# Optimization experiments

Hardware: AMD Instinct MI355X
Metric: run time of the kernel (lower is better)

The kernel has to match this reference:

```python
import jax, jax.numpy as jnp
import numpy as np

M0, M1, M2 = 128, 64, 32            # multiplicities of 0e, 1o, 2e
NUM_IRREPS = M0 + M1 + M2           # 224
NODE_DIM = 128
SPH_DIM = M0 + 3 * M1 + 5 * M2      # 480
HIDDEN = 2 * NODE_DIM + NUM_IRREPS  # 480
N = 100000
EPS = 1e-5
SQ3 = float(np.sqrt(3.0))
SQ5 = float(np.sqrt(5.0))


def _split(x):
    s0 = x[:, :M0]                                   # [N,128]   l=0
    s1 = x[:, M0:M0 + 3 * M1].reshape(-1, M1, 3)     # [N,64,3]  l=1
    s2 = x[:, M0 + 3 * M1:].reshape(-1, M2, 5)       # [N,32,5]  l=2
    return s0, s1, s2


def _merge(s0, s1, s2):
    n = s0.shape[0]
    return jnp.concatenate([s0, s1.reshape(n, -1), s2.reshape(n, -1)], axis=-1)


def _o3_linear(s0, s1, s2, w0, w1, w2, b0):
    # e3nn o3.Linear: one path per l, element path-normalization 1/sqrt(mul_in); bias only on 0e
    y0 = s0 @ w0 / np.float32(np.sqrt(M0)) + b0
    y1 = jnp.einsum('nik,io->nok', s1, w1) / np.float32(np.sqrt(M1))
    y2 = jnp.einsum('nik,io->nok', s2, w2) / np.float32(np.sqrt(M2))
    return y0, y1, y2


def _o3_layernorm(s0, s1, s2, w, b):
    # equivariant layer norm: mean-center scalars only; RMS over (mul, components) per irrep type
    f0 = s0 - jnp.mean(s0, axis=1, keepdims=True)
    n0 = jnp.mean(f0 * f0, axis=1, keepdims=True)
    f0 = f0 * jax.lax.rsqrt(n0 + EPS) * w[:M0] + b
    n1 = jnp.mean(s1 * s1, axis=(1, 2))[:, None, None]
    f1 = s1 * jax.lax.rsqrt(n1 + EPS) * w[M0:M0 + M1][None, :, None]
    n2 = jnp.mean(s2 * s2, axis=(1, 2))[:, None, None]
    f2 = s2 * jax.lax.rsqrt(n2 + EPS) * w[M0 + M1:][None, :, None]
    return f0, f1, f2


def setup_inputs() -> dict:
    key = jax.random.key(0)
    ks = jax.random.split(key, 16)
    g = lambda k, shape: jax.random.normal(k, shape, jnp.float32)
    return {
        'x_scalar': g(ks[0], (N, NODE_DIM)),
        'x_spherical': g(ks[1], (N, SPH_DIM)),
        'ln_g': jnp.ones((NODE_DIM,), jnp.float32),
        'ln_b': jnp.zeros((NODE_DIM,), jnp.float32),
        'o3n_w': jnp.ones((NUM_IRREPS,), jnp.float32),
        'o3n_b': jnp.zeros((M0,), jnp.float32),
        'U_w0': g(ks[2], (M0, M0)), 'U_w1': g(ks[3], (M1, M1)), 'U_w2': g(ks[4], (M2, M2)),
        'U_b0': jnp.zeros((M0,), jnp.float32),
        'V_w0': g(ks[5], (M0, M0)), 'V_w1': g(ks[6], (M1, M1)), 'V_w2': g(ks[7], (M2, M2)),
        'V_b0': jnp.zeros((M0,), jnp.float32),
        'dot_w': g(ks[8], (NUM_IRREPS, NODE_DIM)) / np.float32(np.sqrt(NUM_IRREPS)),
        'mlp_w1': g(ks[9], (NODE_DIM + NUM_IRREPS, NODE_DIM)) / np.float32(np.sqrt(NODE_DIM + NUM_IRREPS)),
        'mlp_b1': jnp.zeros((NODE_DIM,), jnp.float32),
        'mlp_w2': g(ks[10], (NODE_DIM, HIDDEN)) / np.float32(np.sqrt(NODE_DIM)),
        'mlp_b2': jnp.zeros((HIDDEN,), jnp.float32),
    }


def reference(x_scalar, x_spherical, ln_g, ln_b, o3n_w, o3n_b,
              U_w0, U_w1, U_w2, U_b0, V_w0, V_w1, V_w2, V_b0,
              dot_w, mlp_w1, mlp_b1, mlp_w2, mlp_b2):
    # scalar layer norm
    mu = jnp.mean(x_scalar, axis=-1, keepdims=True)
    var = jnp.var(x_scalar, axis=-1, keepdims=True)
    scalar_in = (x_scalar - mu) * jax.lax.rsqrt(var + EPS) * ln_g + ln_b
    # equivariant layer norm on spherical features
    s0, s1, s2 = _split(x_spherical)
    s0, s1, s2 = _o3_layernorm(s0, s1, s2, o3n_w, o3n_b)
    U0, U1, U2 = _o3_linear(s0, s1, s2, U_w0, U_w1, U_w2, U_b0)
    V0, V1, V2 = _o3_linear(s0, s1, s2, V_w0, V_w1, V_w2, V_b0)
    # o3.Norm: per-irrep L2 norm -> [N, 224]
    inv = jnp.concatenate([jnp.abs(V0),
                           jnp.sqrt(jnp.sum(V1 * V1, axis=-1)),
                           jnp.sqrt(jnp.sum(V2 * V2, axis=-1))], axis=-1)
    mlp_in = jnp.concatenate([scalar_in, inv], axis=-1)          # [N, 352]
    h = jax.nn.silu(mlp_in @ mlp_w1 + mlp_b1)
    mlp_out = h @ mlp_w2 + mlp_b2                                # [N, 480]
    a_vv = mlp_out[:, :NUM_IRREPS]
    a_sv = mlp_out[:, NUM_IRREPS:NUM_IRREPS + NODE_DIM]
    a_ss = mlp_out[:, NUM_IRREPS + NODE_DIM:]
    # ElementwiseTensorProduct with 224x0e: per-irrep scalar gating (net factor 1)
    d0 = U0 * a_vv[:, :M0]
    d1 = U1 * a_vv[:, M0:M0 + M1, None]
    d2 = U2 * a_vv[:, M0 + M1:, None]
    # EquivariantDot (component-normalized uuu TP to 0e): dot / sqrt(2l+1)
    dot = jnp.concatenate([U0 * V0,
                           jnp.sum(U1 * V1, axis=-1) / SQ3,
                           jnp.sum(U2 * V2, axis=-1) / SQ5], axis=-1)
    inner = dot @ dot_w                                           # [N, 128]
    d_scalar = a_sv * inner + a_ss
    return x_scalar + d_scalar, x_spherical + _merge(d0, d1, d2)
```

## Files before the change

### kernel.cpp

```cpp
#include <hip/hip_runtime.h>
#include <stdint.h>

typedef unsigned short u16;
typedef __attribute__((ext_vector_type(2))) unsigned short u16x2;
typedef __attribute__((ext_vector_type(4))) unsigned short u16x4;
typedef __attribute__((ext_vector_type(8))) short s16x8;
typedef __attribute__((ext_vector_type(2))) float f32x2;
typedef __attribute__((ext_vector_type(4))) float f32x4;

#define NROWS 100000
#define RPB   16
#define NBLK  (NROWS / RPB)
#define NTHR  512

#define PF   488
#define PS   360
#define PH   136
#define PD   232
#define PAB  484
#define PIF  132

#define OFF_FIN   0
#define OFF_AOUT  0
#define OFF_SCB   15616
#define OFF_INNER 15616
#define OFF_DOTB  27136
#define OFF_HB    34560
#define OFF_BCOM  38912
#define ARENA_SZ  40640

#define B_UW0 0
#define B_UW1 16384
#define B_UW2 20480
#define B_VW0 21504
#define B_VW1 37888
#define B_VW2 41984
#define B_DW  43008
#define B_W1  71680
#define B_W2  116736
#define PACK_TOT 178176

__device__ inline float bf2f(u16 u) {
    union { uint32_t i; float f; } v; v.i = (uint32_t)u << 16; return v.f;
}
__device__ inline u16 f2bf(float f) {
    union { float f; uint32_t i; } v; v.f = f;
    return (u16)((v.i + 0x7fffu + ((v.i >> 16) & 1u)) >> 16);
}
__device__ inline float wsum32(float v) {
    #pragma unroll
    for (int m = 16; m >= 1; m >>= 1) v += __shfl_xor(v, m);
    return v;
}
__device__ inline bool detect_f32(const void* xs) {
    const u16 v = ((const u16*)xs)[threadIdx.x & 63];
    const float f = bf2f(v);
    return __any(!(fabsf(f) < 1e10f)) != 0;
}
__device__ inline float ldin(const void* p, size_t i, bool f32) {
    return f32 ? ((const float*)p)[i] : bf2f(((const u16*)p)[i]);
}
__device__ inline void stout(void* p, size_t i, float v, bool f32) {
    if (f32) ((float*)p)[i] = v; else ((u16*)p)[i] = f2bf(v);
}

struct Ptrs {
    const void *xs, *xp, *lng, *lnb, *o3w, *o3b;
    const void *Uw0, *Uw1, *Uw2, *Ub0, *Vw0, *Vw1, *Vw2, *Vb0;
    const void *dw, *w1, *b1, *w2, *b2;
    const u16 *ws;
    void *out;
};

template<int KS, bool PACKED>
__device__ inline f32x4 mm_acc(const u16* A, int pitchA, const void* W, int D,
                               int tile, int lane, bool wf32)
{
    f32x4 acc = {0.f, 0.f, 0.f, 0.f};
    const int r = lane & 15, g = lane >> 4;
    const u16* arow = A + r * pitchA + g * 8;
    #pragma unroll
    for (int ks = 0; ks < KS; ++ks) {
        s16x8 a = *(const s16x8*)(arow + ks * 32);
        s16x8 b;
        if (PACKED) {
            b = *(const s16x8*)((const u16*)W + (((size_t)tile * KS + ks) * 64 + (size_t)lane) * 8);
        } else {
            union { u16 u[8]; s16x8 v; } bb;
            const int k0 = ks * 32 + g * 8, o = tile * 16 + r;
            #pragma unroll
            for (int j = 0; j < 8; ++j) {
                const size_t idx = (size_t)(k0 + j) * D + o;
                bb.u[j] = wf32 ? f2bf(((const float*)W)[idx]) : ((const u16*)W)[idx];
            }
            b = bb.v;
        }
        acc = __builtin_amdgcn_mfma_f32_16x16x32_bf16(a, b, acc, 0, 0, 0);
    }
    return acc;
}

template<int KS, bool PACKED, int TYPE>
__device__ inline void mm_tile(const u16* A, int pitchA, const void* W, int D,
                               int tile, int lane, float scale, const u16* bias,
                               void* outP, int outPitch, bool wf32)
{
    f32x4 acc = mm_acc<KS, PACKED>(A, pitchA, W, D, tile, lane, wf32);
    const int r = lane & 15, g = lane >> 4;
    const int o = tile * 16 + r;
    if (TYPE == 0) {
        const float bv = bias ? bf2f(bias[o]) : 0.f;
        #pragma unroll
        for (int q = 0; q < 4; ++q)
            ((u16*)outP)[(size_t)(g * 4 + q) * outPitch + o] = f2bf(acc[q] * scale + bv);
    } else if (TYPE == 1) {
        const float bv = bf2f(bias[o]);
        #pragma unroll
        for (int q = 0; q < 4; ++q) {
            float x = acc[q] + bv;
            ((u16*)outP)[(size_t)(g * 4 + q) * outPitch + o] = f2bf(x / (1.f + expf(-x)));
        }
    } else {
        #pragma unroll
        for (int q = 0; q < 4; ++q)
            ((float*)outP)[(size_t)(g * 4 + q) * outPitch + o] = acc[q];
    }
}

__global__ void pack_weights(Ptrs P, u16* ws)
{
    const bool wf32 = detect_f32(P.xs);
    const int gid = blockIdx.x * 256 + threadIdx.x;
    if (gid >= PACK_TOT) return;
    const int  base[10] = {B_UW0, B_UW1, B_UW2, B_VW0, B_VW1, B_VW2, B_DW, B_W1, B_W2, PACK_TOT};
    const int  Kd[9]    = {128, 64, 32, 128, 64, 32, 224, 352, 128};
    const void* srcs[9] = {P.Uw0, P.Uw1, P.Uw2, P.Vw0, P.Vw1, P.Vw2, P.dw, P.w1, P.w2};
    const int  Dstride[9] = {128, 64, 32, 128, 64, 32, 128, 128, 480};
    int m = 0;
    for (int i = 1; i < 9; ++i) if (gid >= base[i]) m = i;
    const int e = gid - base[m];
    const int j = e & 7, lane = (e >> 3) & 63, tk = e >> 9;
    const int Ks = Kd[m] >> 5;
    const int ks = tk % Ks, tile = tk / Ks;
    const int k = ks * 32 + ((lane >> 4) << 3) + j;
    const int o = tile * 16 + (lane & 15);
    const size_t idx = (size_t)k * Dstride[m] + o;
    ws[gid] = wf32 ? f2bf(((const float*)srcs[m])[idx]) : ((const u16*)srcs[m])[idx];
}

template<int DT>
__device__ inline void stage1_core(const Ptrs& P, u16* fin, u16* scb, int tid, int row0)
{
    const int rr = tid >> 5, l32 = tid & 31;
    const size_t row = (size_t)(row0 + rr);
    const u16*   xsb = (const u16*)P.xs + row * 128;
    const float* xsf = (const float*)P.xs + row * 128;
    const u16*   xpb = (const u16*)P.xp + row * 480;
    const float* xpf = (const float*)P.xp + row * 480;
    {
        float v[4];
        if (DT) { f32x4 u = *(const f32x4*)(xsf + l32 * 4); v[0]=u[0];v[1]=u[1];v[2]=u[2];v[3]=u[3]; }
        else    { u16x4 u = *(const u16x4*)(xsb + l32 * 4);
                  v[0]=bf2f(u[0]);v[1]=bf2f(u[1]);v[2]=bf2f(u[2]);v[3]=bf2f(u[3]); }
        float s  = v[0] + v[1] + v[2] + v[3];
        float s2 = v[0]*v[0] + v[1]*v[1] + v[2]*v[2] + v[3]*v[3];
        s = wsum32(s); s2 = wsum32(s2);
        const float mu = s * (1.f / 128.f);
        const float rs = 1.f / sqrtf(s2 * (1.f / 128.f) - mu * mu + 1e-5f);
        const int c = l32 * 4;
        #pragma unroll
        for (int j2 = 0; j2 < 4; ++j2)
            scb[rr * PS + c + j2] =
                f2bf((v[j2] - mu) * rs * ldin(P.lng, c + j2, DT) + ldin(P.lnb, c + j2, DT));
    }
    {
        float v[4];
        if (DT) { f32x4 u = *(const f32x4*)(xpf + l32 * 4); v[0]=u[0];v[1]=u[1];v[2]=u[2];v[3]=u[3]; }
        else    { u16x4 u = *(const u16x4*)(xpb + l32 * 4);
                  v[0]=bf2f(u[0]);v[1]=bf2f(u[1]);v[2]=bf2f(u[2]);v[3]=bf2f(u[3]); }
        float s  = v[0] + v[1] + v[2] + v[3];
        float s2 = v[0]*v[0] + v[1]*v[1] + v[2]*v[2] + v[3]*v[3];
        s = wsum32(s); s2 = wsum32(s2);
        const float mu = s * (1.f / 128.f);
        const float rs = 1.f / sqrtf(s2 * (1.f / 128.f) - mu * mu + 1e-5f);
        const int c = l32 * 4;
        #pragma unroll
        for (int j2 = 0; j2 < 4; ++j2)
            fin[rr * PF + c + j2] =
                f2bf((v[j2] - mu) * rs * ldin(P.o3w, c + j2, DT) + ldin(P.o3b, c + j2, DT));
    }
    {
        const int cb = l32 * 6;
        float w[6];
        if (DT) {
            f32x2 a0 = *(const f32x2*)(xpf + 128 + cb);
            f32x2 a1 = *(const f32x2*)(xpf + 128 + cb + 2);
            f32x2 a2 = *(const f32x2*)(xpf + 128 + cb + 4);
            w[0]=a0[0]; w[1]=a0[1]; w[2]=a1[0]; w[3]=a1[1]; w[4]=a2[0]; w[5]=a2[1];
        } else {
            u16x2 a0 = *(const u16x2*)(xpb + 128 + cb);
            u16x2 a1 = *(const u16x2*)(xpb + 128 + cb + 2);
            u16x2 a2 = *(const u16x2*)(xpb + 128 + cb + 4);
            w[0]=bf2f(a0[0]); w[1]=bf2f(a0[1]); w[2]=bf2f(a1[0]);
            w[3]=bf2f(a1[1]); w[4]=bf2f(a2[0]); w[5]=bf2f(a2[1]);
        }
        float ss = 0.f;
        #pragma unroll
        for (int j2 = 0; j2 < 6; ++j2) ss += w[j2] * w[j2];
        ss = wsum32(ss);
        const float rs = 1.f / sqrtf(ss * (1.f / 192.f) + 1e-5f);
        #pragma unroll
        for (int j2 = 0; j2 < 6; ++j2) {
            const int c = cb + j2, i = c / 3, k = c - 3 * i;
            fin[rr * PF + 128 + k * 64 + i] = f2bf(w[j2] * rs * ldin(P.o3w, 128 + i, DT));
        }
    }
    {
        const int cb = l32 * 5;
        float w[5];
        #pragma unroll
        for (int j2 = 0; j2 < 5; ++j2)
            w[j2] = DT ? xpf[320 + cb + j2] : bf2f(xpb[320 + cb + j2]);
        float ss = 0.f;
        #pragma unroll
        for (int j2 = 0; j2 < 5; ++j2) ss += w[j2] * w[j2];
        ss = wsum32(ss);
        const float rs = 1.f / sqrtf(ss * (1.f / 160.f) + 1e-5f);
        #pragma unroll
        for (int j2 = 0; j2 < 5; ++j2) {
            const int c = cb + j2, i = c / 5, k = c - 5 * i;
            fin[rr * PF + 320 + k * 32 + i] = f2bf(w[j2] * rs * ldin(P.o3w, 192 + i, DT));
        }
    }
}

template<bool PACKED>
__global__ __launch_bounds__(NTHR, 6) void xpainn_main(Ptrs P)
{
    __shared__ __align__(16) unsigned char arena[ARENA_SZ];
    u16*   fin    = (u16*)(arena + OFF_FIN);
    u16*   aoutB  = (u16*)(arena + OFF_AOUT);
    u16*   scb    = (u16*)(arena + OFF_SCB);
    float* innerF = (float*)(arena + OFF_INNER);
    u16*   dotb   = (u16*)(arena + OFF_DOTB);
    u16*   hb     = (u16*)(arena + OFF_HB);
    u16*   bcom   = (u16*)(arena + OFF_BCOM);

    const int tid = threadIdx.x;
    const int lane = tid & 63, wave = tid >> 6;
    const int r = lane & 15, g = lane >> 4;
    const int row0 = blockIdx.x * RPB;
    const bool isf32 = detect_f32(P.xs);

    for (int i = tid; i < 864; i += NTHR) {
        const void* src; int off;
        if (i < 128)      { src = P.Ub0; off = i; }
        else if (i < 256) { src = P.Vb0; off = i - 128; }
        else if (i < 384) { src = P.b1;  off = i - 256; }
        else              { src = P.b2;  off = i - 384; }
        bcom[i] = f2bf(ldin(src, off, isf32));
    }
    if (isf32) stage1_core<1>(P, fin, scb, tid, row0);
    else       stage1_core<0>(P, fin, scb, tid, row0);
    __syncthreads();

    float u0r[4];
    float uxr[5][4];
    {
        const int o = wave * 16 + r;
        f32x4 au = mm_acc<4, PACKED>(fin, PF,
            PACKED ? (const void*)(P.ws + B_UW0) : P.Uw0, 128, wave, lane, isf32);
        f32x4 av = mm_acc<4, PACKED>(fin, PF,
            PACKED ? (const void*)(P.ws + B_VW0) : P.Vw0, 128, wave, lane, isf32);
        const float bu = bf2f(bcom[o]), bv = bf2f(bcom[128 + o]);
        #pragma unroll
        for (int q = 0; q < 4; ++q) {
            const float U = au[q] * 0.08838834764831845f + bu;
            const float V = av[q] * 0.08838834764831845f + bv;
            u0r[q] = U;
            const int row = g * 4 + q;
            scb[row * PS + 128 + o]  = f2bf(fabsf(V));
            dotb[row * PD + o]       = f2bf(U * V);
        }
    }
    if (wave < 4) {
        const int tt = wave, o = tt * 16 + r;
        float sv[4] = {0.f,0.f,0.f,0.f}, suv[4] = {0.f,0.f,0.f,0.f};
        #pragma unroll
        for (int ch = 0; ch < 3; ++ch) {
            f32x4 au = mm_acc<2, PACKED>(fin + 128 + 64 * ch, PF,
                PACKED ? (const void*)(P.ws + B_UW1) : P.Uw1, 64, tt, lane, isf32);
            f32x4 av = mm_acc<2, PACKED>(fin + 128 + 64 * ch, PF,
                PACKED ? (const void*)(P.ws + B_VW1) : P.Vw1, 64, tt, lane, isf32);
            #pragma unroll
            for (int q = 0; q < 4; ++q) {
                const float U = au[q] * 0.125f, V = av[q] * 0.125f;
                uxr[ch][q] = U; sv[q] += V * V; suv[q] += U * V;
            }
        }
        #pragma unroll
        for (int q = 0; q < 4; ++q) {
            const int row = g * 4 + q;
            scb[row * PS + 256 + o]  = f2bf(sqrtf(sv[q]));
            dotb[row * PD + 128 + o] = f2bf(suv[q] * 0.5773502691896258f);
        }
    } else if (wave < 6) {
        const int tt = wave - 4, o = tt * 16 + r;
        float sv[4] = {0.f,0.f,0.f,0.f}, suv[4] = {0.f,0.f,0.f,0.f};
        #pragma unroll
        for (int ch = 0; ch < 5; ++ch) {
            f32x4 au = mm_acc<1, PACKED>(fin + 320 + 32 * ch, PF,
                PACKED ? (const void*)(P.ws + B_UW2) : P.Uw2, 32, tt, lane, isf32);
            f32x4 av = mm_acc<1, PACKED>(fin + 320 + 32 * ch, PF,
                PACKED ? (const void*)(P.ws + B_VW2) : P.Vw2, 32, tt, lane, isf32);
            #pragma unroll
            for (int q = 0; q < 4; ++q) {
                const float U = au[q] * 0.17677669529663687f, V = av[q] * 0.17677669529663687f;
                uxr[ch][q] = U; sv[q] += V * V; suv[q] += U * V;
            }
        }
        #pragma unroll
        for (int q = 0; q < 4; ++q) {
            const int row = g * 4 + q;
            scb[row * PS + 320 + o]  = f2bf(sqrtf(sv[q]));
            dotb[row * PD + 192 + o] = f2bf(suv[q] * 0.4472135954999579f);
        }
    }
    __syncthreads();

    mm_tile<11, PACKED, 1>(scb, PS, PACKED ? (const void*)(P.ws + B_W1) : P.w1,
                           128, wave, lane, 1.f, bcom + 256, hb, PH, isf32);
    __syncthreads();

    for (int ti = wave; ti < 38; ti += 8) {
        if (ti < 30)
            mm_tile<4, PACKED, 0>(hb, PH, PACKED ? (const void*)(P.ws + B_W2) : P.w2,
                                  480, ti, lane, 1.f, bcom + 384, aoutB, PAB, isf32);
        else
            mm_tile<7, PACKED, 2>(dotb, PD, PACKED ? (const void*)(P.ws + B_DW) : P.dw,
                                  128, ti - 30, lane, 1.f, nullptr, innerF, PIF, isf32);
    }
    __syncthreads();

    {
        const int idx = tid;
        const int r2 = idx >> 5, c4 = (idx & 31) * 4;
        const size_t gb = (size_t)(row0 + r2) * 128 + c4;
        const u16x4 asv = *(const u16x4*)(aoutB + r2 * PAB + 224 + c4);
        const u16x4 ass = *(const u16x4*)(aoutB + r2 * PAB + 352 + c4);
        const f32x4 inn = *(const f32x4*)(innerF + r2 * PIF + c4);
        if (isf32) {
            const f32x4 xs = *(const f32x4*)((const float*)P.xs + gb);
            f32x4 o;
            #pragma unroll
            for (int j = 0; j < 4; ++j) o[j] = xs[j] + bf2f(asv[j]) * inn[j] + bf2f(ass[j]);
            *(f32x4*)((float*)P.out + gb) = o;
        } else {
            const u16x4 xs = *(const u16x4*)((const u16*)P.xs + gb);
            u16x4 o;
            #pragma unroll
            for (int j = 0; j < 4; ++j) o[j] = f2bf(bf2f(xs[j]) + bf2f(asv[j]) * inn[j] + bf2f(ass[j]));
            *(u16x4*)((u16*)P.out + gb) = o;
        }
    }
    {
        const size_t ob = (size_t)NROWS * 128;
        const int o = wave * 16 + r;
        #pragma unroll
        for (int q = 0; q < 4; ++q) {
            const int row = g * 4 + q;
            const size_t gr = (size_t)(row0 + row) * 480;
            const float av = bf2f(aoutB[row * PAB + o]);
            stout(P.out, ob + gr + o, ldin(P.xp, gr + o, isf32) + u0r[q] * av, isf32);
        }
        if (wave < 4) {
            const int i = wave * 16 + r;
            #pragma unroll
            for (int q = 0; q < 4; ++q) {
                const int row = g * 4 + q;
                const size_t gr = (size_t)(row0 + row) * 480;
                const float av = bf2f(aoutB[row * PAB + 128 + i]);
                #pragma unroll
                for (int ch = 0; ch < 3; ++ch) {
                    const size_t c = 128 + 3 * i + ch;
                    stout(P.out, ob + gr + c, ldin(P.xp, gr + c, isf32) + uxr[ch][q] * av, isf32);
                }
            }
        } else if (wave < 6) {
            const int i = (wave - 4) * 16 + r;
            #pragma unroll
            for (int q = 0; q < 4; ++q) {
                const int row = g * 4 + q;
                const size_t gr = (size_t)(row0 + row) * 480;
                const float av = bf2f(aoutB[row * PAB + 192 + i]);
                #pragma unroll
                for (int ch = 0; ch < 5; ++ch) {
                    const size_t c = 320 + 5 * i + ch;
                    stout(P.out, ob + gr + c, ldin(P.xp, gr + c, isf32) + uxr[ch][q] * av, isf32);
                }
            }
        }
    }
}

extern "C" void kernel_launch(void* const* d_in, const int* in_sizes, int n_in,
                              void* d_out, int out_size, void* d_ws, size_t ws_size,
                              hipStream_t stream)
{
    Ptrs P;
    P.xs  = d_in[0];  P.xp  = d_in[1];
    P.lng = d_in[2];  P.lnb = d_in[3];
    P.o3w = d_in[4];  P.o3b = d_in[5];
    P.Uw0 = d_in[6];  P.Uw1 = d_in[7];
    P.Uw2 = d_in[8];  P.Ub0 = d_in[9];
    P.Vw0 = d_in[10]; P.Vw1 = d_in[11];
    P.Vw2 = d_in[12]; P.Vb0 = d_in[13];
    P.dw  = d_in[14]; P.w1  = d_in[15];
    P.b1  = d_in[16]; P.w2  = d_in[17];
    P.b2  = d_in[18];
    P.ws  = (const u16*)d_ws;
    P.out = d_out;

    const bool packed = (ws_size >= (size_t)PACK_TOT * sizeof(u16));
    if (packed) {
        pack_weights<<<(PACK_TOT + 255) / 256, 256, 0, stream>>>(P, (u16*)d_ws);
        xpainn_main<true><<<NBLK, NTHR, 0, stream>>>(P);
    } else {
        xpainn_main<false><<<NBLK, NTHR, 0, stream>>>(P);
    }
}
```

Measured before the change: 244.3 us.

## Process 32 rows per block and reuse weight fragments across two row groups

Doubles rows per block from 16 to 32, splitting the shared-memory arena into two 16-row groups. Each weight B-fragment is now loaded into registers once and applied to both row groups' MFMAs, halving weight-load traffic per row. The costs are double the LDS footprint (about 79.5KB), a launch-bounds occupancy hint lowered from 6 to 4, and more live registers for the per-group U values, which may reduce latency hiding. 100000 rows still divide evenly into 32-row blocks.

```diff
diff --git a/kernel.cpp b/kernel.cpp
--- a/kernel.cpp
+++ b/kernel.cpp
@@ -9,7 +9,7 @@
 typedef __attribute__((ext_vector_type(4))) float f32x4;
 
 #define NROWS 100000
-#define RPB   16
+#define RPB   32
 #define NBLK  (NROWS / RPB)
 #define NTHR  512
 
@@ -19,15 +19,21 @@
 #define PD   232
 #define PAB  484
 #define PIF  132
+#define FIN_RG  (16 * PF)
+#define SCB_RG  (16 * PS)
+#define HB_RG   (16 * PH)
+#define DOT_RG  (16 * PD)
+#define AOUT_RG (16 * PAB)
+#define INN_RG  (16 * PIF)
 
 #define OFF_FIN   0
 #define OFF_AOUT  0
-#define OFF_SCB   15616
-#define OFF_INNER 15616
-#define OFF_DOTB  27136
-#define OFF_HB    34560
-#define OFF_BCOM  38912
-#define ARENA_SZ  40640
+#define OFF_SCB   31232
+#define OFF_INNER 31232
+#define OFF_DOTB  54272
+#define OFF_HB    69120
+#define OFF_BCOM  77824
+#define ARENA_SZ  79552
 
 #define B_UW0 0
 #define B_UW1 16384
@@ -73,57 +79,52 @@
 };
 
 template<int KS, bool PACKED>
-__device__ inline f32x4 mm_acc(const u16* A, int pitchA, const void* W, int D,
-                               int tile, int lane, bool wf32)
-{
-    f32x4 acc = {0.f, 0.f, 0.f, 0.f};
-    const int r = lane & 15, g = lane >> 4;
-    const u16* arow = A + r * pitchA + g * 8;
+__device__ inline void load_b(const void* W, int D, int tile, int lane, bool wf32, s16x8* bfr)
+{
     #pragma unroll
     for (int ks = 0; ks < KS; ++ks) {
-        s16x8 a = *(const s16x8*)(arow + ks * 32);
-        s16x8 b;
         if (PACKED) {
-            b = *(const s16x8*)((const u16*)W + (((size_t)tile * KS + ks) * 64 + (size_t)lane) * 8);
+            bfr[ks] = *(const s16x8*)((const u16*)W + (((size_t)tile * KS + ks) * 64 + (size_t)lane) * 8);
         } else {
             union { u16 u[8]; s16x8 v; } bb;
-            const int k0 = ks * 32 + g * 8, o = tile * 16 + r;
+            const int k0 = ks * 32 + ((lane >> 4) << 3), o = tile * 16 + (lane & 15);
             #pragma unroll
             for (int j = 0; j < 8; ++j) {
                 const size_t idx = (size_t)(k0 + j) * D + o;
                 bb.u[j] = wf32 ? f2bf(((const float*)W)[idx]) : ((const u16*)W)[idx];
             }
-            b = bb.v;
-        }
-        acc = __builtin_amdgcn_mfma_f32_16x16x32_bf16(a, b, acc, 0, 0, 0);
+            bfr[ks] = bb.v;
+        }
+    }
+}
+
+template<int KS>
+__device__ inline f32x4 acc_ab(const u16* A, int pitchA, int lane, const s16x8* bfr)
+{
+    f32x4 acc = {0.f, 0.f, 0.f, 0.f};
+    const u16* arow = A + (lane & 15) * pitchA + (lane >> 4) * 8;
+    #pragma unroll
+    for (int ks = 0; ks < KS; ++ks) {
+        s16x8 a = *(const s16x8*)(arow + ks * 32);
+        acc = __builtin_amdgcn_mfma_f32_16x16x32_bf16(a, bfr[ks], acc, 0, 0, 0);
     }
     return acc;
 }
 
-template<int KS, bool PACKED, int TYPE>
-__device__ inline void mm_tile(const u16* A, int pitchA, const void* W, int D,
-                               int tile, int lane, float scale, const u16* bias,
-                               void* outP, int outPitch, bool wf32)
-{
-    f32x4 acc = mm_acc<KS, PACKED>(A, pitchA, W, D, tile, lane, wf32);
+template<int KS, bool PACKED>
+__device__ inline void mm_silu(const u16* A, int pitchA, const void* W, int D,
+                               int tile, int lane, const u16* bias, u16* outH, bool wf32)
+{
+    s16x8 bfr[KS];
+    load_b<KS, PACKED>(W, D, tile, lane, wf32, bfr);
+    f32x4 acc = acc_ab<KS>(A, pitchA, lane, bfr);
     const int r = lane & 15, g = lane >> 4;
     const int o = tile * 16 + r;
-    if (TYPE == 0) {
-        const float bv = bias ? bf2f(bias[o]) : 0.f;
-        #pragma unroll
-        for (int q = 0; q < 4; ++q)
-            ((u16*)outP)[(size_t)(g * 4 + q) * outPitch + o] = f2bf(acc[q] * scale + bv);
-    } else if (TYPE == 1) {
-        const float bv = bf2f(bias[o]);
-        #pragma unroll
-        for (int q = 0; q < 4; ++q) {
-            float x = acc[q] + bv;
-            ((u16*)outP)[(size_t)(g * 4 + q) * outPitch + o] = f2bf(x / (1.f + expf(-x)));
-        }
-    } else {
-        #pragma unroll
-        for (int q = 0; q < 4; ++q)
-            ((float*)outP)[(size_t)(g * 4 + q) * outPitch + o] = acc[q];
+    const float bv = bf2f(bias[o]);
+    #pragma unroll
+    for (int q = 0; q < 4; ++q) {
+        float x = acc[q] + bv;
+        outH[(g * 4 + q) * PH + o] = f2bf(x / (1.f + expf(-x)));
     }
 }
 
@@ -149,93 +150,99 @@
 }
 
 template<int DT>
-__device__ inline void stage1_core(const Ptrs& P, u16* fin, u16* scb, int tid, int row0)
-{
-    const int rr = tid >> 5, l32 = tid & 31;
-    const size_t row = (size_t)(row0 + rr);
-    const u16*   xsb = (const u16*)P.xs + row * 128;
-    const float* xsf = (const float*)P.xs + row * 128;
-    const u16*   xpb = (const u16*)P.xp + row * 480;
-    const float* xpf = (const float*)P.xp + row * 480;
-    {
-        float v[4];
-        if (DT) { f32x4 u = *(const f32x4*)(xsf + l32 * 4); v[0]=u[0];v[1]=u[1];v[2]=u[2];v[3]=u[3]; }
-        else    { u16x4 u = *(const u16x4*)(xsb + l32 * 4);
-                  v[0]=bf2f(u[0]);v[1]=bf2f(u[1]);v[2]=bf2f(u[2]);v[3]=bf2f(u[3]); }
-        float s  = v[0] + v[1] + v[2] + v[3];
-        float s2 = v[0]*v[0] + v[1]*v[1] + v[2]*v[2] + v[3]*v[3];
-        s = wsum32(s); s2 = wsum32(s2);
-        const float mu = s * (1.f / 128.f);
-        const float rs = 1.f / sqrtf(s2 * (1.f / 128.f) - mu * mu + 1e-5f);
-        const int c = l32 * 4;
-        #pragma unroll
-        for (int j2 = 0; j2 < 4; ++j2)
-            scb[rr * PS + c + j2] =
-                f2bf((v[j2] - mu) * rs * ldin(P.lng, c + j2, DT) + ldin(P.lnb, c + j2, DT));
-    }
-    {
-        float v[4];
-        if (DT) { f32x4 u = *(const f32x4*)(xpf + l32 * 4); v[0]=u[0];v[1]=u[1];v[2]=u[2];v[3]=u[3]; }
-        else    { u16x4 u = *(const u16x4*)(xpb + l32 * 4);
-                  v[0]=bf2f(u[0]);v[1]=bf2f(u[1]);v[2]=bf2f(u[2]);v[3]=bf2f(u[3]); }
-        float s  = v[0] + v[1] + v[2] + v[3];
-        float s2 = v[0]*v[0] + v[1]*v[1] + v[2]*v[2] + v[3]*v[3];
-        s = wsum32(s); s2 = wsum32(s2);
-        const float mu = s * (1.f / 128.f);
-        const float rs = 1.f / sqrtf(s2 * (1.f / 128.f) - mu * mu + 1e-5f);
-        const int c = l32 * 4;
-        #pragma unroll
-        for (int j2 = 0; j2 < 4; ++j2)
-            fin[rr * PF + c + j2] =
-                f2bf((v[j2] - mu) * rs * ldin(P.o3w, c + j2, DT) + ldin(P.o3b, c + j2, DT));
-    }
-    {
-        const int cb = l32 * 6;
-        float w[6];
-        if (DT) {
-            f32x2 a0 = *(const f32x2*)(xpf + 128 + cb);
-            f32x2 a1 = *(const f32x2*)(xpf + 128 + cb + 2);
-            f32x2 a2 = *(const f32x2*)(xpf + 128 + cb + 4);
-            w[0]=a0[0]; w[1]=a0[1]; w[2]=a1[0]; w[3]=a1[1]; w[4]=a2[0]; w[5]=a2[1];
-        } else {
-            u16x2 a0 = *(const u16x2*)(xpb + 128 + cb);
-            u16x2 a1 = *(const u16x2*)(xpb + 128 + cb + 2);
-            u16x2 a2 = *(const u16x2*)(xpb + 128 + cb + 4);
-            w[0]=bf2f(a0[0]); w[1]=bf2f(a0[1]); w[2]=bf2f(a1[0]);
-            w[3]=bf2f(a1[1]); w[4]=bf2f(a2[0]); w[5]=bf2f(a2[1]);
-        }
-        float ss = 0.f;
-        #pragma unroll
-        for (int j2 = 0; j2 < 6; ++j2) ss += w[j2] * w[j2];
-        ss = wsum32(ss);
-        const float rs = 1.f / sqrtf(ss * (1.f / 192.f) + 1e-5f);
-        #pragma unroll
-        for (int j2 = 0; j2 < 6; ++j2) {
-            const int c = cb + j2, i = c / 3, k = c - 3 * i;
-            fin[rr * PF + 128 + k * 64 + i] = f2bf(w[j2] * rs * ldin(P.o3w, 128 + i, DT));
-        }
-    }
-    {
-        const int cb = l32 * 5;
-        float w[5];
-        #pragma unroll
-        for (int j2 = 0; j2 < 5; ++j2)
-            w[j2] = DT ? xpf[320 + cb + j2] : bf2f(xpb[320 + cb + j2]);
-        float ss = 0.f;
-        #pragma unroll
-        for (int j2 = 0; j2 < 5; ++j2) ss += w[j2] * w[j2];
-        ss = wsum32(ss);
-        const float rs = 1.f / sqrtf(ss * (1.f / 160.f) + 1e-5f);
-        #pragma unroll
-        for (int j2 = 0; j2 < 5; ++j2) {
-            const int c = cb + j2, i = c / 5, k = c - 5 * i;
-            fin[rr * PF + 320 + k * 32 + i] = f2bf(w[j2] * rs * ldin(P.o3w, 192 + i, DT));
+__device__ inline void stage1_core(const Ptrs& P, u16* fin0, u16* scb0, int tid, int row0)
+{
+    const int hw = tid >> 5, l32 = tid & 31;
+    #pragma unroll
+    for (int rg = 0; rg < 2; ++rg) {
+        const int rr = hw + rg * 16;
+        const size_t row = (size_t)(row0 + rr);
+        u16* finr = fin0 + rg * FIN_RG + hw * PF;
+        u16* scbr = scb0 + rg * SCB_RG + hw * PS;
+        const u16*   xsb = (const u16*)P.xs + row * 128;
+        const float* xsf = (const float*)P.xs + row * 128;
+        const u16*   xpb = (const u16*)P.xp + row * 480;
+        const float* xpf = (const float*)P.xp + row * 480;
+        {
+            float v[4];
+            if (DT) { f32x4 u = *(const f32x4*)(xsf + l32 * 4); v[0]=u[0];v[1]=u[1];v[2]=u[2];v[3]=u[3]; }
+            else    { u16x4 u = *(const u16x4*)(xsb + l32 * 4);
+                      v[0]=bf2f(u[0]);v[1]=bf2f(u[1]);v[2]=bf2f(u[2]);v[3]=bf2f(u[3]); }
+            float s  = v[0] + v[1] + v[2] + v[3];
+            float s2 = v[0]*v[0] + v[1]*v[1] + v[2]*v[2] + v[3]*v[3];
+            s = wsum32(s); s2 = wsum32(s2);
+            const float mu = s * (1.f / 128.f);
+            const float rs = 1.f / sqrtf(s2 * (1.f / 128.f) - mu * mu + 1e-5f);
+            const int c = l32 * 4;
+            #pragma unroll
+            for (int j2 = 0; j2 < 4; ++j2)
+                scbr[c + j2] =
+                    f2bf((v[j2] - mu) * rs * ldin(P.lng, c + j2, DT) + ldin(P.lnb, c + j2, DT));
+        }
+        {
+            float v[4];
+            if (DT) { f32x4 u = *(const f32x4*)(xpf + l32 * 4); v[0]=u[0];v[1]=u[1];v[2]=u[2];v[3]=u[3]; }
+            else    { u16x4 u = *(const u16x4*)(xpb + l32 * 4);
+                      v[0]=bf2f(u[0]);v[1]=bf2f(u[1]);v[2]=bf2f(u[2]);v[3]=bf2f(u[3]); }
+            float s  = v[0] + v[1] + v[2] + v[3];
+            float s2 = v[0]*v[0] + v[1]*v[1] + v[2]*v[2] + v[3]*v[3];
+            s = wsum32(s); s2 = wsum32(s2);
+            const float mu = s * (1.f / 128.f);
+            const float rs = 1.f / sqrtf(s2 * (1.f / 128.f) - mu * mu + 1e-5f);
+            const int c = l32 * 4;
+            #pragma unroll
+            for (int j2 = 0; j2 < 4; ++j2)
+                finr[c + j2] =
+                    f2bf((v[j2] - mu) * rs * ldin(P.o3w, c + j2, DT) + ldin(P.o3b, c + j2, DT));
+        }
+        {
+            const int cb = l32 * 6;
+            float w[6];
+            if (DT) {
+                f32x2 a0 = *(const f32x2*)(xpf + 128 + cb);
+                f32x2 a1 = *(const f32x2*)(xpf + 128 + cb + 2);
+                f32x2 a2 = *(const f32x2*)(xpf + 128 + cb + 4);
+                w[0]=a0[0]; w[1]=a0[1]; w[2]=a1[0]; w[3]=a1[1]; w[4]=a2[0]; w[5]=a2[1];
+            } else {
+                u16x2 a0 = *(const u16x2*)(xpb + 128 + cb);
+                u16x2 a1 = *(const u16x2*)(xpb + 128 + cb + 2);
+                u16x2 a2 = *(const u16x2*)(xpb + 128 + cb + 4);
+                w[0]=bf2f(a0[0]); w[1]=bf2f(a0[1]); w[2]=bf2f(a1[0]);
+                w[3]=bf2f(a1[1]); w[4]=bf2f(a2[0]); w[5]=bf2f(a2[1]);
+            }
+            float ss = 0.f;
+            #pragma unroll
+            for (int j2 = 0; j2 < 6; ++j2) ss += w[j2] * w[j2];
+            ss = wsum32(ss);
+            const float rs = 1.f / sqrtf(ss * (1.f / 192.f) + 1e-5f);
+            #pragma unroll
+            for (int j2 = 0; j2 < 6; ++j2) {
+                const int c = cb + j2, i = c / 3, k = c - 3 * i;
+                finr[128 + k * 64 + i] = f2bf(w[j2] * rs * ldin(P.o3w, 128 + i, DT));
+            }
+        }
+        {
+            const int cb = l32 * 5;
+            float w[5];
+            #pragma unroll
+            for (int j2 = 0; j2 < 5; ++j2)
+                w[j2] = DT ? xpf[320 + cb + j2] : bf2f(xpb[320 + cb + j2]);
+            float ss = 0.f;
+            #pragma unroll
+            for (int j2 = 0; j2 < 5; ++j2) ss += w[j2] * w[j2];
+            ss = wsum32(ss);
+            const float rs = 1.f / sqrtf(ss * (1.f / 160.f) + 1e-5f);
+            #pragma unroll
+            for (int j2 = 0; j2 < 5; ++j2) {
+                const int c = cb + j2, i = c / 5, k = c - 5 * i;
+                finr[320 + k * 32 + i] = f2bf(w[j2] * rs * ldin(P.o3w, 192 + i, DT));
+            }
         }
     }
 }
 
 template<bool PACKED>
-__global__ __launch_bounds__(NTHR, 6) void xpainn_main(Ptrs P)
+__global__ __launch_bounds__(NTHR, 4) void xpainn_main(Ptrs P)
 {
     __shared__ __align__(16) unsigned char arena[ARENA_SZ];
     u16*   fin    = (u16*)(arena + OFF_FIN);
@@ -264,91 +271,138 @@
     else       stage1_core<0>(P, fin, scb, tid, row0);
     __syncthreads();
 
-    float u0r[4];
-    float uxr[5][4];
+    float u0r[2][4];
+    float uxr[2][5][4];
     {
+        s16x8 bU[4], bV[4];
+        load_b<4, PACKED>(PACKED ? (const void*)(P.ws + B_UW0) : P.Uw0, 128, wave, lane, isf32, bU);
+        load_b<4, PACKED>(PACKED ? (const void*)(P.ws + B_VW0) : P.Vw0, 128, wave, lane, isf32, bV);
         const int o = wave * 16 + r;
-        f32x4 au = mm_acc<4, PACKED>(fin, PF,
-            PACKED ? (const void*)(P.ws + B_UW0) : P.Uw0, 128, wave, lane, isf32);
-        f32x4 av = mm_acc<4, PACKED>(fin, PF,
-            PACKED ? (const void*)(P.ws + B_VW0) : P.Vw0, 128, wave, lane, isf32);
         const float bu = bf2f(bcom[o]), bv = bf2f(bcom[128 + o]);
         #pragma unroll
-        for (int q = 0; q < 4; ++q) {
-            const float U = au[q] * 0.08838834764831845f + bu;
-            const float V = av[q] * 0.08838834764831845f + bv;
-            u0r[q] = U;
-            const int row = g * 4 + q;
-            scb[row * PS + 128 + o]  = f2bf(fabsf(V));
-            dotb[row * PD + o]       = f2bf(U * V);
+        for (int rg = 0; rg < 2; ++rg) {
+            f32x4 au = acc_ab<4>(fin + rg * FIN_RG, PF, lane, bU);
+            f32x4 av = acc_ab<4>(fin + rg * FIN_RG, PF, lane, bV);
+            u16* scbR = scb + rg * SCB_RG;
+            u16* dotR = dotb + rg * DOT_RG;
+            #pragma unroll
+            for (int q = 0; q < 4; ++q) {
+                const float U = au[q] * 0.08838834764831845f + bu;
+                const float V = av[q] * 0.08838834764831845f + bv;
+                u0r[rg][q] = U;
+                const int lrow = g * 4 + q;
+                scbR[lrow * PS + 128 + o] = f2bf(fabsf(V));
+                dotR[lrow * PD + o]       = f2bf(U * V);
+            }
         }
     }
     if (wave < 4) {
         const int tt = wave, o = tt * 16 + r;
-        float sv[4] = {0.f,0.f,0.f,0.f}, suv[4] = {0.f,0.f,0.f,0.f};
+        float sv[2][4] = {{0.f,0.f,0.f,0.f},{0.f,0.f,0.f,0.f}};
+        float suv[2][4] = {{0.f,0.f,0.f,0.f},{0.f,0.f,0.f,0.f}};
         #pragma unroll
         for (int ch = 0; ch < 3; ++ch) {
-            f32x4 au = mm_acc<2, PACKED>(fin + 128 + 64 * ch, PF,
-                PACKED ? (const void*)(P.ws + B_UW1) : P.Uw1, 64, tt, lane, isf32);
-            f32x4 av = mm_acc<2, PACKED>(fin + 128 + 64 * ch, PF,
-                PACKED ? (const void*)(P.ws + B_VW1) : P.Vw1, 64, tt, lane, isf32);
+            s16x8 bU[2], bV[2];
+            load_b<2, PACKED>(PACKED ? (const void*)(P.ws + B_UW1) : P.Uw1, 64, tt, lane, isf32, bU);
+            load_b<2, PACKED>(PACKED ? (const void*)(P.ws + B_VW1) : P.Vw1, 64, tt, lane, isf32, bV);
+            #pragma unroll
+            for (int rg = 0; rg < 2; ++rg) {
+                f32x4 au = acc_ab<2>(fin + rg * FIN_RG + 128 + 64 * ch, PF, lane, bU);
+                f32x4 av = acc_ab<2>(fin + rg * FIN_RG + 128 + 64 * ch, PF, lane, bV);
+                #pragma unroll
+                for (int q = 0; q < 4; ++q) {
+                    const float U = au[q] * 0.125f, V = av[q] * 0.125f;
+                    uxr[rg][ch][q] = U; sv[rg][q] += V * V; suv[rg][q] += U * V;
+                }
+            }
+        }
+        #pragma unroll
+        for (int rg = 0; rg < 2; ++rg) {
             #pragma unroll
             for (int q = 0; q < 4; ++q) {
-                const float U = au[q] * 0.125f, V = av[q] * 0.125f;
-                uxr[ch][q] = U; sv[q] += V * V; suv[q] += U * V;
-            }
-        }
-        #pragma unroll
-        for (int q = 0; q < 4; ++q) {
-            const int row = g * 4 + q;
-            scb[row * PS + 256 + o]  = f2bf(sqrtf(sv[q]));
-            dotb[row * PD + 128 + o] = f2bf(suv[q] * 0.5773502691896258f);
+                const int lrow = g * 4 + q;
+                (scb + rg * SCB_RG)[lrow * PS + 256 + o]  = f2bf(sqrtf(sv[rg][q]));
+                (dotb + rg * DOT_RG)[lrow * PD + 128 + o] = f2bf(suv[rg][q] * 0.5773502691896258f);
+            }
         }
     } else if (wave < 6) {
         const int tt = wave - 4, o = tt * 16 + r;
-        float sv[4] = {0.f,0.f,0.f,0.f}, suv[4] = {0.f,0.f,0.f,0.f};
+        float sv[2][4] = {{0.f,0.f,0.f,0.f},{0.f,0.f,0.f,0.f}};
+        float suv[2][4] = {{0.f,0.f,0.f,0.f},{0.f,0.f,0.f,0.f}};
         #pragma unroll
         for (int ch = 0; ch < 5; ++ch) {
-            f32x4 au = mm_acc<1, PACKED>(fin + 320 + 32 * ch, PF,
-                PACKED ? (const void*)(P.ws + B_UW2) : P.Uw2, 32, tt, lane, isf32);
-            f32x4 av = mm_acc<1, PACKED>(fin + 320 + 32 * ch, PF,
-                PACKED ? (const void*)(P.ws + B_VW2) : P.Vw2, 32, tt, lane, isf32);
+            s16x8 bU[1], bV[1];
+            load_b<1, PACKED>(PACKED ? (const void*)(P.ws + B_UW2) : P.Uw2, 32, tt, lane, isf32, bU);
+            load_b<1, PACKED>(PACKED ? (const void*)(P.ws + B_VW2) : P.Vw2, 32, tt, lane, isf32, bV);
+            #pragma unroll
+            for (int rg = 0; rg < 2; ++rg) {
+                f32x4 au = acc_ab<1>(fin + rg * FIN_RG + 320 + 32 * ch, PF, lane, bU);
+                f32x4 av = acc_ab<1>(fin + rg * FIN_RG + 320 + 32 * ch, PF, lane, bV);
+                #pragma unroll
+                for (int q = 0; q < 4; ++q) {
+                    const float U = au[q] * 0.17677669529663687f, V = av[q] * 0.17677669529663687f;
+                    uxr[rg][ch][q] = U; sv[rg][q] += V * V; suv[rg][q] += U * V;
+                }
+            }
+        }
+        #pragma unroll
+        for (int rg = 0; rg < 2; ++rg) {
             #pragma unroll
             for (int q = 0; q < 4; ++q) {
-                const float U = au[q] * 0.17677669529663687f, V = av[q] * 0.17677669529663687f;
-                uxr[ch][q] = U; sv[q] += V * V; suv[q] += U * V;
-            }
-        }
-        #pragma unroll
-        for (int q = 0; q < 4; ++q) {
-            const int row = g * 4 + q;
-            scb[row * PS + 320 + o]  = f2bf(sqrtf(sv[q]));
-            dotb[row * PD + 192 + o] = f2bf(suv[q] * 0.4472135954999579f);
+                const int lrow = g * 4 + q;
+                (scb + rg * SCB_RG)[lrow * PS + 320 + o]  = f2bf(sqrtf(sv[rg][q]));
+                (dotb + rg * DOT_RG)[lrow * PD + 192 + o] = f2bf(suv[rg][q] * 0.4472135954999579f);
+            }
         }
     }
     __syncthreads();
 
-    mm_tile<11, PACKED, 1>(scb, PS, PACKED ? (const void*)(P.ws + B_W1) : P.w1,
-                           128, wave, lane, 1.f, bcom + 256, hb, PH, isf32);
+    #pragma unroll
+    for (int rg = 0; rg < 2; ++rg)
+        mm_silu<11, PACKED>(scb + rg * SCB_RG, PS, PACKED ? (const void*)(P.ws + B_W1) : P.w1,
+                            128, wave, lane, bcom + 256, hb + rg * HB_RG, isf32);
     __syncthreads();
 
     for (int ti = wave; ti < 38; ti += 8) {
-        if (ti < 30)
-            mm_tile<4, PACKED, 0>(hb, PH, PACKED ? (const void*)(P.ws + B_W2) : P.w2,
-                                  480, ti, lane, 1.f, bcom + 384, aoutB, PAB, isf32);
-        else
-            mm_tile<7, PACKED, 2>(dotb, PD, PACKED ? (const void*)(P.ws + B_DW) : P.dw,
-                                  128, ti - 30, lane, 1.f, nullptr, innerF, PIF, isf32);
+        if (ti < 30) {
+            s16x8 bfr[4];
+            load_b<4, PACKED>(PACKED ? (const void*)(P.ws + B_W2) : P.w2, 480, ti, lane, isf32, bfr);
+            const int o = ti * 16 + r;
+            const float bv = bf2f(bcom[384 + o]);
+            #pragma unroll
+            for (int rg = 0; rg < 2; ++rg) {
+                f32x4 acc = acc_ab<4>(hb + rg * HB_RG, PH, lane, bfr);
+                u16* aoutR = aoutB + rg * AOUT_RG;
+                #pragma unroll
+                for (int q = 0; q < 4; ++q)
+                    aoutR[(g * 4 + q) * PAB + o] = f2bf(acc[q] + bv);
+            }
+        } else {
+            s16x8 bfr[7];
+            load_b<7, PACKED>(PACKED ? (const void*)(P.ws + B_DW) : P.dw, 128, ti - 30, lane, isf32, bfr);
+            const int o = (ti - 30) * 16 + r;
+            #pragma unroll
+            for (int rg = 0; rg < 2; ++rg) {
+                f32x4 acc = acc_ab<7>(dotb + rg * DOT_RG, PD, lane, bfr);
+                float* innR = innerF + rg * INN_RG;
+                #pragma unroll
+                for (int q = 0; q < 4; ++q)
+                    innR[(g * 4 + q) * PIF + o] = acc[q];
+            }
+        }
     }
     __syncthreads();
 
-    {
-        const int idx = tid;
+    #pragma unroll
+    for (int it = 0; it < 2; ++it) {
+        const int idx = tid + it * NTHR;
         const int r2 = idx >> 5, c4 = (idx & 31) * 4;
+        const u16*  aoutR = aoutB + (r2 >> 4) * AOUT_RG + (r2 & 15) * PAB;
+        const float* innR = innerF + (r2 >> 4) * INN_RG + (r2 & 15) * PIF;
         const size_t gb = (size_t)(row0 + r2) * 128 + c4;
-        const u16x4 asv = *(const u16x4*)(aoutB + r2 * PAB + 224 + c4);
-        const u16x4 ass = *(const u16x4*)(aoutB + r2 * PAB + 352 + c4);
-        const f32x4 inn = *(const f32x4*)(innerF + r2 * PIF + c4);
+        const u16x4 asv = *(const u16x4*)(aoutR + 224 + c4);
+        const u16x4 ass = *(const u16x4*)(aoutR + 352 + c4);
+        const f32x4 inn = *(const f32x4*)(innR + c4);
         if (isf32) {
             const f32x4 xs = *(const f32x4*)((const float*)P.xs + gb);
             f32x4 o;
@@ -365,38 +419,42 @@
     }
     {
         const size_t ob = (size_t)NROWS * 128;
-        const int o = wave * 16 + r;
-        #pragma unroll
-        for (int q = 0; q < 4; ++q) {
-            const int row = g * 4 + q;
-            const size_t gr = (size_t)(row0 + row) * 480;
-            const float av = bf2f(aoutB[row * PAB + o]);
-            stout(P.out, ob + gr + o, ldin(P.xp, gr + o, isf32) + u0r[q] * av, isf32);
-        }
-        if (wave < 4) {
-            const int i = wave * 16 + r;
+        #pragma unroll
+        for (int rg = 0; rg < 2; ++rg) {
+            const u16* aoutR = aoutB + rg * AOUT_RG;
+            const int o = wave * 16 + r;
             #pragma unroll
             for (int q = 0; q < 4; ++q) {
-                const int row = g * 4 + q;
-                const size_t gr = (size_t)(row0 + row) * 480;
-                const float av = bf2f(aoutB[row * PAB + 128 + i]);
-                #pragma unroll
-                for (int ch = 0; ch < 3; ++ch) {
-                    const size_t c = 128 + 3 * i + ch;
-                    stout(P.out, ob + gr + c, ldin(P.xp, gr + c, isf32) + uxr[ch][q] * av, isf32);
+                const int lrow = g * 4 + q;
+                const size_t gr = (size_t)(row0 + rg * 16 + lrow) * 480;
+                const float av = bf2f(aoutR[lrow * PAB + o]);
+                stout(P.out, ob + gr + o, ldin(P.xp, gr + o, isf32) + u0r[rg][q] * av, isf32);
+            }
+            if (wave < 4) {
+                const int i = wave * 16 + r;
+                #pragma unroll
+                for (int q = 0; q < 4; ++q) {
+                    const int lrow = g * 4 + q;
+                    const size_t gr = (size_t)(row0 + rg * 16 + lrow) * 480;
+                    const float av = bf2f(aoutR[lrow * PAB + 128 + i]);
+                    #pragma unroll
+                    for (int ch = 0; ch < 3; ++ch) {
+                        const size_t c = 128 + 3 * i + ch;
+                        stout(P.out, ob + gr + c, ldin(P.xp, gr + c, isf32) + uxr[rg][ch][q] * av, isf32);
+                    }
                 }
-            }
-        } else if (wave < 6) {
-            const int i = (wave - 4) * 16 + r;
-            #pragma unroll
-            for (int q = 0; q < 4; ++q) {
-                const int row = g * 4 + q;
-                const size_t gr = (size_t)(row0 + row) * 480;
-                const float av = bf2f(aoutB[row * PAB + 192 + i]);
-                #pragma unroll
-                for (int ch = 0; ch < 5; ++ch) {
-                    const size_t c = 320 + 5 * i + ch;
-                    stout(P.out, ob + gr + c, ldin(P.xp, gr + c, isf32) + uxr[ch][q] * av, isf32);
+            } else if (wave < 6) {
+                const int i = (wave - 4) * 16 + r;
+                #pragma unroll
+                for (int q = 0; q < 4; ++q) {
+                    const int lrow = g * 4 + q;
+                    const size_t gr = (size_t)(row0 + rg * 16 + lrow) * 480;
+                    const float av = bf2f(aoutR[lrow * PAB + 192 + i]);
+                    #pragma unroll
+                    for (int ch = 0; ch < 5; ++ch) {
+                        const size_t c = 320 + 5 * i + ch;
+                        stout(P.out, ob + gr + c, ldin(P.xp, gr + c, isf32) + uxr[rg][ch][q] * av, isf32);
+                    }
                 }
             }
         }
```

New measurement: 235.9 us. 1.04x faster.
